# Performance work log

Measured on AMD Instinct MI355X. Metric: run time of the kernel, lower is better.

Reference implementation:

```python
import jax, jax.numpy as jnp
import numpy as np

IH = IW = 1024          # image size (iH, iW)
NMS_CAND = 1000         # dup_attrs['nms_candidates']
NMS_THR = 0.65          # dup_attrs['nms_thr']
MAX_SEGS = 100          # max_segs


def _mask_to_box(masks):
    # masks: [N, H, W] bool -> xyxy float boxes [N, 4] in pixel coords
    N, H, W = masks.shape
    rows = masks.any(axis=2)            # [N, H]
    cols = masks.any(axis=1)            # [N, W]
    x1 = jnp.argmax(cols, axis=1)
    x2 = W - jnp.argmax(cols[:, ::-1], axis=1)
    y1 = jnp.argmax(rows, axis=1)
    y2 = H - jnp.argmax(rows[:, ::-1], axis=1)
    return jnp.stack([x1, y1, x2, y2], axis=-1).astype(jnp.float32)


def _box_iou(b):
    # b: [K, 4] xyxy -> pairwise IoU [K, K]
    x1, y1, x2, y2 = b[:, 0], b[:, 1], b[:, 2], b[:, 3]
    area = (x2 - x1) * (y2 - y1)
    ix1 = jnp.maximum(x1[:, None], x1[None, :])
    iy1 = jnp.maximum(y1[:, None], y1[None, :])
    ix2 = jnp.minimum(x2[:, None], x2[None, :])
    iy2 = jnp.minimum(y2[:, None], y2[None, :])
    inter = jnp.clip(ix2 - ix1, 0.0) * jnp.clip(iy2 - iy1, 0.0)
    union = area[:, None] + area[None, :] - inter
    return inter / jnp.maximum(union, 1e-9)


def _greedy_nms_keep(iou, thr):
    # boxes assumed pre-sorted by descending score; returns keep mask [K]
    k = iou.shape[0]
    idx = jnp.arange(k)

    def body(i, keep):
        sup = keep[i] & (iou[i] > thr) & (idx > i)
        return keep & ~sup

    return jax.lax.fori_loop(0, k, body, jnp.ones((k,), dtype=bool))


def setup_inputs() -> dict:
    key = jax.random.key(0)
    k1, k2 = jax.random.split(key)
    cls_logits = jax.random.normal(k1, (300, 81), dtype=jnp.float32)
    seg_logits = jax.random.normal(k2, (300, 200, 200), dtype=jnp.float32)
    return {"cls_logits": cls_logits, "seg_logits": seg_logits}


def reference(cls_logits, seg_logits):
    N, fH, fW = seg_logits.shape
    C = cls_logits.shape[1] - 1  # last class is background/no-object

    # mask thresholding + emptiness flag (filtering replaced by score masking)
    pred_masks = seg_logits > 0                              # [N, fH, fW]
    non_empty = pred_masks.reshape(N, -1).sum(axis=1) > 0    # [N]

    # mask -> box for NMS
    boxes = _mask_to_box(pred_masks)                         # [N, 4]

    # sigmoid scoring over (feat, class); empty masks get score -1 (never picked)
    scores = jax.nn.sigmoid(cls_logits[:, :-1])              # [N, C]
    scores = jnp.where(non_empty[:, None], scores, -1.0).reshape(-1)  # [N*C]
    feat_ids = jnp.repeat(jnp.arange(N), C)                  # [N*C]
    labels = jnp.tile(jnp.arange(C), N)                      # [N*C]

    # top nms_candidates (scores sorted descending)
    k = min(NMS_CAND, N * C)
    cand_scores, cand_ids = jax.lax.top_k(scores, k)
    cand_feats = feat_ids[cand_ids]
    cand_labels = labels[cand_ids]
    cand_boxes = boxes[cand_feats]

    # batched (class-aware) NMS: offset boxes per label
    offset = cand_labels.astype(jnp.float32)[:, None] * (float(max(fH, fW)) + 1.0)
    iou = _box_iou(cand_boxes + offset)
    keep = _greedy_nms_keep(iou, NMS_THR) & (cand_scores >= 0.0)

    # keep top max_segs among survivors
    kept_scores = jnp.where(keep, cand_scores, -jnp.inf)
    sel_scores, sel = jax.lax.top_k(kept_scores, MAX_SEGS)
    sel_feats = cand_feats[sel]
    sel_labels = cand_labels[sel]

    # upsample selected mask logits to image size and threshold
    sel_logits = seg_logits[sel_feats]                       # [M, fH, fW]
    maps = jax.image.resize(sel_logits, (MAX_SEGS, IH, IW), method='bilinear')
    out_masks = maps > 0                                     # [M, iH, iW] bool
    batch_ids = jnp.zeros((MAX_SEGS,), dtype=jnp.int32)

    return sel_labels, out_masks, sel_scores, batch_ids
```

## Files before the change

kernel.cpp:

```cpp
#include <hip/hip_runtime.h>
#include <cstdint>
#include <cstddef>

typedef unsigned int u32;
typedef unsigned long long u64;
typedef float vf4 __attribute__((ext_vector_type(4)));

#define NF 300
#define NCLS 80
#define NCLS1 81
#define FH 200
#define FW 200
#define PIX 40000
#define NC 24000
#define KCAND 1000
#define CAP 4096
#define NBINS 65536
#define MAXSEG 100
#define OUT_MASK_OFF 100
#define OUT_SCORE_OFF 104857700
#define OUT_BATCH_OFF 104857800
#define NEG_BIG -3.3895313892515355e38f
#define RYC 16

#define WS_HIST      0u
#define WS_KEYS      262144u
#define WS_COLLECT   454144u
#define WS_CNT       486912u
#define WS_BOXES     486928u
#define WS_CLAB      496928u
#define WS_CFEAT     500928u
#define WS_CSCORE    504928u
#define WS_CBOX      508928u
#define WS_ROWBITS   524928u
#define WS_SELFEAT   656128u
#define WS_WTAB      656528u
#define WS_KEEP      672912u

__device__ __forceinline__ u32 ord32_r3(float f) {
  u32 b = __float_as_uint(f);
  return (b & 0x80000000u) ? ~b : (b | 0x80000000u);
}
__device__ __forceinline__ float unord32_r3(u32 o) {
  u32 b = (o & 0x80000000u) ? (o & 0x7FFFFFFFu) : ~o;
  return __uint_as_float(b);
}

__global__ void r3_init_wtab(u32* __restrict__ hist, u32* __restrict__ cnts,
                             float4* __restrict__ wtab) {
  int i = blockIdx.x * 256 + threadIdx.x;
  hist[i] = 0u;
  if (i < 4) cnts[i] = 0u;
  if (i < 1024) {
    float s = __fsub_rn(__fmul_rn((float)i + 0.5f, 0.1953125f), 0.5f);
    int j0 = (int)floorf(s);
    int j1 = j0 + 1;
    float w0 = fmaxf(0.f, __fsub_rn(1.f, fabsf(__fsub_rn(s, (float)j0))));
    float w1 = fmaxf(0.f, __fsub_rn(1.f, fabsf(__fsub_rn(s, (float)j1))));
    bool in0 = (j0 >= 0) && (j0 < FH);
    bool in1 = (j1 >= 0) && (j1 < FH);
    float tot = __fadd_rn(in0 ? w0 : 0.f, in1 ? w1 : 0.f);
    float w0n = in0 ? (w0 / tot) : 0.f;
    float w1n = in1 ? (w1 / tot) : 0.f;
    wtab[i] = make_float4(w0n, w1n, (float)max(j0, 0), (float)min(j1, FH - 1));
  }
}

__global__ void r3_boxes_scores(const float* __restrict__ seg, const float* __restrict__ cls,
                                float4* __restrict__ boxes, u64* __restrict__ keys,
                                u32* __restrict__ hist) {
  __shared__ int sminx[256], sminy[256], smaxx[256], smaxy[256];
  int n = blockIdx.x, t = threadIdx.x;
  const float4* img = (const float4*)(seg + (size_t)n * PIX);
  int minx = FW, miny = FH, maxx = -1, maxy = -1;
  for (int q = t; q < PIX / 4; q += 256) {
    float4 v = img[q];
    int p = q * 4;
    int y = p / FW;
    int x = p - y * FW;
    if (v.x > 0.f) { minx = min(minx, x);     maxx = max(maxx, x);     miny = min(miny, y); maxy = max(maxy, y); }
    if (v.y > 0.f) { minx = min(minx, x + 1); maxx = max(maxx, x + 1); miny = min(miny, y); maxy = max(maxy, y); }
    if (v.z > 0.f) { minx = min(minx, x + 2); maxx = max(maxx, x + 2); miny = min(miny, y); maxy = max(maxy, y); }
    if (v.w > 0.f) { minx = min(minx, x + 3); maxx = max(maxx, x + 3); miny = min(miny, y); maxy = max(maxy, y); }
  }
  sminx[t] = minx; sminy[t] = miny; smaxx[t] = maxx; smaxy[t] = maxy;
  __syncthreads();
  for (int s = 128; s > 0; s >>= 1) {
    if (t < s) {
      sminx[t] = min(sminx[t], sminx[t + s]);
      sminy[t] = min(sminy[t], sminy[t + s]);
      smaxx[t] = max(smaxx[t], smaxx[t + s]);
      smaxy[t] = max(smaxy[t], smaxy[t + s]);
    }
    __syncthreads();
  }
  bool ne = smaxx[0] >= 0;
  if (t == 0) {
    float4 b;
    if (ne) b = make_float4((float)sminx[0], (float)sminy[0], (float)(smaxx[0] + 1), (float)(smaxy[0] + 1));
    else    b = make_float4(0.f, 0.f, (float)FW, (float)FH);
    boxes[n] = b;
  }
  if (t < NCLS) {
    float sc;
    if (ne) {
      float lg = cls[n * NCLS1 + t];
      sc = 1.0f / (1.0f + expf(-lg));
    } else {
      sc = -1.0f;
    }
    u32 o = ord32_r3(sc);
    u32 i = (u32)(n * NCLS + t);
    keys[i] = ((u64)o << 32) | (u64)(0xFFFFFFFFu - i);
    atomicAdd(&hist[o >> 16], 1u);
  }
}

__global__ void r3_thresh(const u32* __restrict__ hist, u32* __restrict__ cnts) {
  __shared__ u32 s[1024];
  int t = threadIdx.x;
  u32 sum = 0;
  const u32* hp = hist + t * 64;
  for (int b = 0; b < 64; b++) sum += hp[b];
  s[t] = sum;
  __syncthreads();
  for (int off = 1; off < 1024; off <<= 1) {
    u32 v = s[t];
    u32 o = (t + off < 1024) ? s[t + off] : 0u;
    __syncthreads();
    s[t] = v + o;
    __syncthreads();
  }
  u32 sufnext = (t < 1023) ? s[t + 1] : 0u;
  if (s[t] >= (u32)KCAND && sufnext < (u32)KCAND) {
    u32 run = sufnext;
    u32 B = (u32)(t * 64);
    for (int b = 63; b >= 0; b--) {
      run += hist[t * 64 + b];
      if (run >= (u32)KCAND) { B = (u32)(t * 64 + b); break; }
    }
    cnts[1] = B;
  }
}

__global__ void r3_collect(const u64* __restrict__ keys, const u32* __restrict__ cnts,
                           u64* __restrict__ collect, u32* __restrict__ counter) {
  int i = blockIdx.x * 256 + threadIdx.x;
  if (i >= NC) return;
  u64 k = keys[i];
  if ((u32)(k >> 48) >= cnts[1]) {
    u32 pos = atomicAdd(counter, 1u);
    if (pos < CAP) collect[pos] = k;
  }
}

__global__ void r3_rank(const u64* __restrict__ collect, const u32* __restrict__ cnts,
                        const float4* __restrict__ boxes,
                        int* __restrict__ clab, int* __restrict__ cfeat,
                        float* __restrict__ cscore, float4* __restrict__ cbox) {
  __shared__ u64 sk[CAP];
  int M = min((int)cnts[0], CAP);
  int t = threadIdx.x;
  for (int j = t; j < M; j += 64) sk[j] = collect[j];
  __syncthreads();
  for (int j = blockIdx.x * 64 + t; j < M; j += 64 * 16) {
    u64 mykey = sk[j];
    int r = 0;
    for (int k = 0; k < M; k++) r += (sk[k] > mykey) ? 1 : 0;
    if (r < KCAND) {
      u32 idx = 0xFFFFFFFFu - (u32)(mykey & 0xFFFFFFFFull);
      int n = (int)idx / NCLS, c = (int)idx - n * NCLS;
      clab[r] = c;
      cfeat[r] = n;
      cscore[r] = unord32_r3((u32)(mykey >> 32));
      float4 b = boxes[n];
      float off = (float)c * 201.0f;
      cbox[r] = make_float4(b.x + off, b.y + off, b.z + off, b.w + off);
    }
  }
}

__global__ void r3_iou(const float4* __restrict__ cbox, u64* __restrict__ rowbits) {
  int i = blockIdx.x;
  int lane = threadIdx.x;
  float4 bi = make_float4(0.f, 0.f, 0.f, 0.f);
  float ai = 0.f;
  if (i < KCAND) { bi = cbox[i]; ai = (bi.z - bi.x) * (bi.w - bi.y); }
  for (int ch = 0; ch < 16; ch++) {
    int j = ch * 64 + lane;
    bool pred = false;
    if (i < KCAND && j < KCAND && j > i) {
      float4 bj = cbox[j];
      float aj = (bj.z - bj.x) * (bj.w - bj.y);
      float ix1 = fmaxf(bi.x, bj.x), iy1 = fmaxf(bi.y, bj.y);
      float ix2 = fminf(bi.z, bj.z), iy2 = fminf(bi.w, bj.w);
      float inter = fmaxf(ix2 - ix1, 0.f) * fmaxf(iy2 - iy1, 0.f);
      float uni = ai + aj - inter;
      float iou = inter / fmaxf(uni, 1e-9f);
      pred = iou > 0.65f;
    }
    u64 m = __ballot(pred);
    if (lane == 0) rowbits[(size_t)i * 16 + ch] = m;
  }
}

__global__ void r3_nms(const u64* __restrict__ rowbits, u64* __restrict__ keepout) {
  __shared__ u64 sup[16];
  __shared__ u64 keep[16];
  int t = threadIdx.x;
  if (t < 16) sup[t] = 0ull;
  __syncthreads();
  for (int c = 0; c < 16; c++) {
    int L = t;
    u64 r = rowbits[(size_t)(c * 64 + L) * 16 + c];
    u64 s = sup[c];
    u64 k = 0ull;
    #pragma unroll 4
    for (int b = 0; b < 64; b++) {
      u64 rb = __shfl(r, b, 64);
      if (!((s >> b) & 1ull)) { s |= rb; k |= (1ull << b); }
    }
    if (L == 0) { sup[c] = s; keep[c] = k; }
    if (L > c && L < 16) {
      u64 acc = sup[L];
      #pragma unroll
      for (int b = 0; b < 64; b++) {
        u64 v = rowbits[(size_t)(c * 64 + b) * 16 + L];
        if ((k >> b) & 1ull) acc |= v;
      }
      sup[L] = acc;
    }
    __syncthreads();
  }
  if (t < 16) keepout[t] = keep[t];
}

__global__ void r3_sel(const u64* __restrict__ keepbits, const float* __restrict__ cscore,
                       const int* __restrict__ clab, const int* __restrict__ cfeat,
                       float* __restrict__ out, int* __restrict__ selfeat) {
  __shared__ u64 sk[KCAND];
  __shared__ u64 kb[16];
  int t = threadIdx.x;
  if (t < 16) kb[t] = keepbits[t];
  __syncthreads();
  for (int j = t; j < KCAND; j += 64) {
    bool kp = ((kb[j >> 6] >> (j & 63)) & 1ull) != 0ull;
    float sc = cscore[j];
    u32 hi = (kp && sc >= 0.f) ? ord32_r3(sc) : 0u;
    sk[j] = ((u64)hi << 32) | (u64)(0xFFFFFFFFu - (u32)j);
  }
  __syncthreads();
  int j = blockIdx.x * 64 + t;
  if (j < KCAND) {
    u64 my = sk[j];
    int r = 0;
    for (int k = 0; k < KCAND; k++) r += (sk[k] > my) ? 1 : 0;
    if (r < MAXSEG) {
      u32 hi = (u32)(my >> 32);
      float oscore = (hi == 0u) ? NEG_BIG : unord32_r3(hi);
      oscore = fmaxf(oscore, NEG_BIG);
      out[r] = (float)clab[j];
      out[OUT_SCORE_OFF + r] = oscore;
      out[OUT_BATCH_OFF + r] = 0.0f;
      selfeat[r] = cfeat[j];
    }
  }
}

__global__ void __launch_bounds__(256) r3_resize(const float* __restrict__ seg,
                                                 const int* __restrict__ selfeat,
                                                 const float4* __restrict__ wtab,
                                                 float* __restrict__ outm) {
  __shared__ float srow[6][FW];
  int t = threadIdx.x;
  int yb = blockIdx.x * RYC, slot = blockIdx.y;
  int feat = selfeat[slot];
  const float* img = seg + (size_t)feat * PIX;
  float4 wxa = wtab[t * 4], wxb = wtab[t * 4 + 1], wxc = wtab[t * 4 + 2], wxd = wtab[t * 4 + 3];
  int ylo = (int)wtab[yb].z;
  int yhi = (int)wtab[yb + RYC - 1].w;
  int nr = yhi - ylo + 1;
  for (int e = t; e < nr * FW; e += 256) {
    int rr = e / FW, cc = e - rr * FW;
    srow[rr][cc] = img[(ylo + rr) * FW + cc];
  }
  __syncthreads();
  int xb = t * 4;
  int xa0 = (int)wxa.z, xa1 = (int)wxa.w;
  int xb0 = (int)wxb.z, xb1 = (int)wxb.w;
  int xc0 = (int)wxc.z, xc1 = (int)wxc.w;
  int xd0 = (int)wxd.z, xd1 = (int)wxd.w;
  float* obase = outm + (size_t)slot * 1048576 + (size_t)yb * 1024 + xb;
  #pragma unroll
  for (int r = 0; r < RYC; r++) {
    int y = yb + r;
    float4 wy = wtab[y];
    const float* r0 = srow[(int)wy.z - ylo];
    const float* r1 = srow[(int)wy.w - ylo];
    float wy0 = wy.x, wy1 = wy.y;
    float ta0 = __fmaf_rn(wy1, r1[xa0], __fmul_rn(wy0, r0[xa0]));
    float ta1 = __fmaf_rn(wy1, r1[xa1], __fmul_rn(wy0, r0[xa1]));
    float va  = __fmaf_rn(wxa.y, ta1, __fmul_rn(wxa.x, ta0));
    float tb0 = __fmaf_rn(wy1, r1[xb0], __fmul_rn(wy0, r0[xb0]));
    float tb1 = __fmaf_rn(wy1, r1[xb1], __fmul_rn(wy0, r0[xb1]));
    float vb  = __fmaf_rn(wxb.y, tb1, __fmul_rn(wxb.x, tb0));
    float tc0 = __fmaf_rn(wy1, r1[xc0], __fmul_rn(wy0, r0[xc0]));
    float tc1 = __fmaf_rn(wy1, r1[xc1], __fmul_rn(wy0, r0[xc1]));
    float vc  = __fmaf_rn(wxc.y, tc1, __fmul_rn(wxc.x, tc0));
    float td0 = __fmaf_rn(wy1, r1[xd0], __fmul_rn(wy0, r0[xd0]));
    float td1 = __fmaf_rn(wy1, r1[xd1], __fmul_rn(wy0, r0[xd1]));
    float vd  = __fmaf_rn(wxd.y, td1, __fmul_rn(wxd.x, td0));
    vf4 res;
    res.x = (va > 0.0f) ? 1.0f : 0.0f;
    res.y = (vb > 0.0f) ? 1.0f : 0.0f;
    res.z = (vc > 0.0f) ? 1.0f : 0.0f;
    res.w = (vd > 0.0f) ? 1.0f : 0.0f;
    *(vf4*)(obase + (size_t)r * 1024) = res;
  }
}

extern "C" void kernel_launch(void* const* d_in, const int* in_sizes, int n_in,
                              void* d_out, int out_size, void* d_ws, size_t ws_size,
                              hipStream_t stream) {
  const float* cls = (const float*)d_in[0];
  const float* seg = (const float*)d_in[1];
  float* out = (float*)d_out;
  char* ws = (char*)d_ws;

  u32* hist      = (u32*)(ws + WS_HIST);
  u64* keys      = (u64*)(ws + WS_KEYS);
  u64* collect   = (u64*)(ws + WS_COLLECT);
  u32* cnts      = (u32*)(ws + WS_CNT);
  float4* boxes  = (float4*)(ws + WS_BOXES);
  int* clab      = (int*)(ws + WS_CLAB);
  int* cfeat     = (int*)(ws + WS_CFEAT);
  float* cscore  = (float*)(ws + WS_CSCORE);
  float4* cbox   = (float4*)(ws + WS_CBOX);
  u64* rowbits   = (u64*)(ws + WS_ROWBITS);
  int* selfeat   = (int*)(ws + WS_SELFEAT);
  float4* wtab   = (float4*)(ws + WS_WTAB);
  u64* keepbits  = (u64*)(ws + WS_KEEP);

  r3_init_wtab<<<dim3(NBINS / 256), dim3(256), 0, stream>>>(hist, cnts, wtab);
  r3_boxes_scores<<<dim3(NF), dim3(256), 0, stream>>>(seg, cls, boxes, keys, hist);
  r3_thresh<<<dim3(1), dim3(1024), 0, stream>>>(hist, cnts);
  r3_collect<<<dim3((NC + 255) / 256), dim3(256), 0, stream>>>(keys, cnts, collect, &cnts[0]);
  r3_rank<<<dim3(16), dim3(64), 0, stream>>>(collect, cnts, boxes, clab, cfeat, cscore, cbox);
  r3_iou<<<dim3(1024), dim3(64), 0, stream>>>(cbox, rowbits);
  r3_nms<<<dim3(1), dim3(64), 0, stream>>>(rowbits, keepbits);
  r3_sel<<<dim3(16), dim3(64), 0, stream>>>(keepbits, cscore, clab, cfeat, out, selfeat);
  r3_resize<<<dim3(1024 / RYC, MAXSEG), dim3(256), 0, stream>>>(seg, selfeat, wtab, out + OUT_MASK_OFF);
}
```

Measured before the change: 642.3 us.

## Fuse NMS with selection, inline resize weights, widen small pipeline kernels

Merges the NMS and top-100 selection kernels into one 1024-thread kernel. Selection now uses a ballot and prefix-popcount compaction instead of an O(K^2) rank comparison. The bilinear weight table is dropped and weights are recomputed inline in the resize kernel, removing its table-fill work and global table loads. Collect switches to wave-aggregated atomics, rank uses 256-thread blocks so all candidates are covered in one pass, and the IoU kernel stages boxes in shared memory with four rows per block. The aim is fewer launches and less serial latency in the small control stages, at the cost of extra ALU work per resize thread.

```diff
diff --git a/kernel.cpp b/kernel.cpp
--- a/kernel.cpp
+++ b/kernel.cpp
@@ -34,8 +34,6 @@
 #define WS_CBOX      508928u
 #define WS_ROWBITS   524928u
 #define WS_SELFEAT   656128u
-#define WS_WTAB      656528u
-#define WS_KEEP      672912u
 
 __device__ __forceinline__ u32 ord32_r3(float f) {
   u32 b = __float_as_uint(f);
@@ -46,29 +44,29 @@
   return __uint_as_float(b);
 }
 
-__global__ void r3_init_wtab(u32* __restrict__ hist, u32* __restrict__ cnts,
-                             float4* __restrict__ wtab) {
+__device__ __forceinline__ float4 wcalc_r4(int i) {
+  float s = __fsub_rn(__fmul_rn((float)i + 0.5f, 0.1953125f), 0.5f);
+  int j0 = (int)floorf(s);
+  int j1 = j0 + 1;
+  float w0 = fmaxf(0.f, __fsub_rn(1.f, fabsf(__fsub_rn(s, (float)j0))));
+  float w1 = fmaxf(0.f, __fsub_rn(1.f, fabsf(__fsub_rn(s, (float)j1))));
+  bool in0 = (j0 >= 0) && (j0 < FH);
+  bool in1 = (j1 >= 0) && (j1 < FH);
+  float tot = __fadd_rn(in0 ? w0 : 0.f, in1 ? w1 : 0.f);
+  float w0n = in0 ? (w0 / tot) : 0.f;
+  float w1n = in1 ? (w1 / tot) : 0.f;
+  return make_float4(w0n, w1n, (float)max(j0, 0), (float)min(j1, FH - 1));
+}
+
+__global__ void r5_init(u32* __restrict__ hist, u32* __restrict__ cnts) {
   int i = blockIdx.x * 256 + threadIdx.x;
   hist[i] = 0u;
   if (i < 4) cnts[i] = 0u;
-  if (i < 1024) {
-    float s = __fsub_rn(__fmul_rn((float)i + 0.5f, 0.1953125f), 0.5f);
-    int j0 = (int)floorf(s);
-    int j1 = j0 + 1;
-    float w0 = fmaxf(0.f, __fsub_rn(1.f, fabsf(__fsub_rn(s, (float)j0))));
-    float w1 = fmaxf(0.f, __fsub_rn(1.f, fabsf(__fsub_rn(s, (float)j1))));
-    bool in0 = (j0 >= 0) && (j0 < FH);
-    bool in1 = (j1 >= 0) && (j1 < FH);
-    float tot = __fadd_rn(in0 ? w0 : 0.f, in1 ? w1 : 0.f);
-    float w0n = in0 ? (w0 / tot) : 0.f;
-    float w1n = in1 ? (w1 / tot) : 0.f;
-    wtab[i] = make_float4(w0n, w1n, (float)max(j0, 0), (float)min(j1, FH - 1));
-  }
-}
-
-__global__ void r3_boxes_scores(const float* __restrict__ seg, const float* __restrict__ cls,
-                                float4* __restrict__ boxes, u64* __restrict__ keys,
-                                u32* __restrict__ hist) {
+}
+
+__global__ void r5_boxes(const float* __restrict__ seg, const float* __restrict__ cls,
+                         float4* __restrict__ boxes, u64* __restrict__ keys,
+                         u32* __restrict__ hist) {
   __shared__ int sminx[256], sminy[256], smaxx[256], smaxy[256];
   int n = blockIdx.x, t = threadIdx.x;
   const float4* img = (const float4*)(seg + (size_t)n * PIX);
@@ -116,7 +114,7 @@
   }
 }
 
-__global__ void r3_thresh(const u32* __restrict__ hist, u32* __restrict__ cnts) {
+__global__ void r5_thresh(const u32* __restrict__ hist, u32* __restrict__ cnts) {
   __shared__ u32 s[1024];
   int t = threadIdx.x;
   u32 sum = 0;
@@ -143,36 +141,47 @@
   }
 }
 
-__global__ void r3_collect(const u64* __restrict__ keys, const u32* __restrict__ cnts,
+__global__ void r5_collect(const u64* __restrict__ keys, const u32* __restrict__ cnts,
                            u64* __restrict__ collect, u32* __restrict__ counter) {
   int i = blockIdx.x * 256 + threadIdx.x;
-  if (i >= NC) return;
-  u64 k = keys[i];
-  if ((u32)(k >> 48) >= cnts[1]) {
-    u32 pos = atomicAdd(counter, 1u);
+  u32 B = cnts[1];
+  bool pass = false;
+  u64 k = 0ull;
+  if (i < NC) {
+    k = keys[i];
+    pass = ((u32)(k >> 48) >= B);
+  }
+  u64 m = __ballot(pass);
+  int lane = threadIdx.x & 63;
+  u32 base = 0u;
+  if (lane == 0 && m) base = atomicAdd(counter, (u32)__popcll(m));
+  base = __shfl(base, 0, 64);
+  if (pass) {
+    u32 pos = base + (u32)__popcll(m & ((1ull << lane) - 1ull));
     if (pos < CAP) collect[pos] = k;
   }
 }
 
-__global__ void r3_rank(const u64* __restrict__ collect, const u32* __restrict__ cnts,
+__global__ void r5_rank(const u64* __restrict__ collect, const u32* __restrict__ cnts,
                         const float4* __restrict__ boxes,
                         int* __restrict__ clab, int* __restrict__ cfeat,
                         float* __restrict__ cscore, float4* __restrict__ cbox) {
   __shared__ u64 sk[CAP];
   int M = min((int)cnts[0], CAP);
   int t = threadIdx.x;
-  for (int j = t; j < M; j += 64) sk[j] = collect[j];
-  __syncthreads();
-  for (int j = blockIdx.x * 64 + t; j < M; j += 64 * 16) {
-    u64 mykey = sk[j];
+  for (int j = t; j < M; j += 256) sk[j] = collect[j];
+  __syncthreads();
+  int j = blockIdx.x * 256 + t;
+  if (j < M) {
+    u64 my = sk[j];
     int r = 0;
-    for (int k = 0; k < M; k++) r += (sk[k] > mykey) ? 1 : 0;
+    for (int k = 0; k < M; k++) r += (sk[k] > my) ? 1 : 0;
     if (r < KCAND) {
-      u32 idx = 0xFFFFFFFFu - (u32)(mykey & 0xFFFFFFFFull);
+      u32 idx = 0xFFFFFFFFu - (u32)(my & 0xFFFFFFFFull);
       int n = (int)idx / NCLS, c = (int)idx - n * NCLS;
       clab[r] = c;
       cfeat[r] = n;
-      cscore[r] = unord32_r3((u32)(mykey >> 32));
+      cscore[r] = unord32_r3((u32)(my >> 32));
       float4 b = boxes[n];
       float off = (float)c * 201.0f;
       cbox[r] = make_float4(b.x + off, b.y + off, b.z + off, b.w + off);
@@ -180,17 +189,21 @@
   }
 }
 
-__global__ void r3_iou(const float4* __restrict__ cbox, u64* __restrict__ rowbits) {
-  int i = blockIdx.x;
-  int lane = threadIdx.x;
+__global__ void r5_iou(const float4* __restrict__ cbox, u64* __restrict__ rowbits) {
+  __shared__ float4 sb[KCAND];
+  int t = threadIdx.x;
+  for (int j = t; j < KCAND; j += 256) sb[j] = cbox[j];
+  __syncthreads();
+  int w = t >> 6, lane = t & 63;
+  int i = blockIdx.x * 4 + w;
   float4 bi = make_float4(0.f, 0.f, 0.f, 0.f);
   float ai = 0.f;
-  if (i < KCAND) { bi = cbox[i]; ai = (bi.z - bi.x) * (bi.w - bi.y); }
+  if (i < KCAND) { bi = sb[i]; ai = (bi.z - bi.x) * (bi.w - bi.y); }
   for (int ch = 0; ch < 16; ch++) {
     int j = ch * 64 + lane;
     bool pred = false;
     if (i < KCAND && j < KCAND && j > i) {
-      float4 bj = cbox[j];
+      float4 bj = sb[j];
       float aj = (bj.z - bj.x) * (bj.w - bj.y);
       float ix1 = fmaxf(bi.x, bj.x), iy1 = fmaxf(bi.y, bj.y);
       float ix2 = fminf(bi.z, bj.z), iy2 = fminf(bi.w, bj.w);
@@ -204,81 +217,86 @@
   }
 }
 
-__global__ void r3_nms(const u64* __restrict__ rowbits, u64* __restrict__ keepout) {
+__global__ void r5_nms_sel(const u64* __restrict__ rowbits, const float* __restrict__ cscore,
+                           const int* __restrict__ clab, const int* __restrict__ cfeat,
+                           float* __restrict__ out, int* __restrict__ selfeat) {
   __shared__ u64 sup[16];
   __shared__ u64 keep[16];
+  __shared__ u64 sel[16];
+  __shared__ u32 pre[17];
   int t = threadIdx.x;
   if (t < 16) sup[t] = 0ull;
   __syncthreads();
   for (int c = 0; c < 16; c++) {
-    int L = t;
-    u64 r = rowbits[(size_t)(c * 64 + L) * 16 + c];
-    u64 s = sup[c];
-    u64 k = 0ull;
-    #pragma unroll 4
-    for (int b = 0; b < 64; b++) {
-      u64 rb = __shfl(r, b, 64);
-      if (!((s >> b) & 1ull)) { s |= rb; k |= (1ull << b); }
-    }
-    if (L == 0) { sup[c] = s; keep[c] = k; }
-    if (L > c && L < 16) {
-      u64 acc = sup[L];
-      #pragma unroll
+    if (t < 64) {
+      int L = t;
+      u64 r = rowbits[(size_t)(c * 64 + L) * 16 + c];
+      u64 s = sup[c];
+      u64 k = 0ull;
+      #pragma unroll 4
       for (int b = 0; b < 64; b++) {
-        u64 v = rowbits[(size_t)(c * 64 + b) * 16 + L];
-        if ((k >> b) & 1ull) acc |= v;
+        u64 rb = __shfl(r, b, 64);
+        if (!((s >> b) & 1ull)) { s |= rb; k |= (1ull << b); }
       }
-      sup[L] = acc;
+      if (L == 0) { sup[c] = s; keep[c] = k; }
+      if (L > c && L < 16) {
+        u64 acc = sup[L];
+        #pragma unroll
+        for (int b = 0; b < 64; b++) {
+          u64 v = rowbits[(size_t)(c * 64 + b) * 16 + L];
+          if ((k >> b) & 1ull) acc |= v;
+        }
+        sup[L] = acc;
+      }
     }
     __syncthreads();
   }
-  if (t < 16) keepout[t] = keep[t];
-}
-
-__global__ void r3_sel(const u64* __restrict__ keepbits, const float* __restrict__ cscore,
-                       const int* __restrict__ clab, const int* __restrict__ cfeat,
-                       float* __restrict__ out, int* __restrict__ selfeat) {
-  __shared__ u64 sk[KCAND];
-  __shared__ u64 kb[16];
-  int t = threadIdx.x;
-  if (t < 16) kb[t] = keepbits[t];
-  __syncthreads();
-  for (int j = t; j < KCAND; j += 64) {
-    bool kp = ((kb[j >> 6] >> (j & 63)) & 1ull) != 0ull;
-    float sc = cscore[j];
-    u32 hi = (kp && sc >= 0.f) ? ord32_r3(sc) : 0u;
-    sk[j] = ((u64)hi << 32) | (u64)(0xFFFFFFFFu - (u32)j);
-  }
-  __syncthreads();
-  int j = blockIdx.x * 64 + t;
-  if (j < KCAND) {
-    u64 my = sk[j];
-    int r = 0;
-    for (int k = 0; k < KCAND; k++) r += (sk[k] > my) ? 1 : 0;
+  {
+    int w = t >> 6, lane = t & 63;
+    bool s = false;
+    if (t < KCAND) {
+      bool kp = ((keep[t >> 6] >> (t & 63)) & 1ull) != 0ull;
+      s = kp && (cscore[t] >= 0.f);
+    }
+    u64 m = __ballot(s);
+    if (lane == 0) sel[w] = m;
+  }
+  __syncthreads();
+  if (t == 0) {
+    u32 acc = 0;
+    #pragma unroll
+    for (int c = 0; c < 16; c++) { pre[c] = acc; acc += (u32)__popcll(sel[c]); }
+    pre[16] = acc;
+  }
+  __syncthreads();
+  u32 nkept = pre[16];
+  if (t < KCAND) {
+    int j = t;
+    u64 w = sel[j >> 6];
+    bool s = ((w >> (j & 63)) & 1ull) != 0ull;
+    u32 below = pre[j >> 6] + (u32)__popcll(w & ((1ull << (j & 63)) - 1ull));
+    u32 r = s ? below : (nkept + (u32)j - below);
     if (r < MAXSEG) {
-      u32 hi = (u32)(my >> 32);
-      float oscore = (hi == 0u) ? NEG_BIG : unord32_r3(hi);
-      oscore = fmaxf(oscore, NEG_BIG);
       out[r] = (float)clab[j];
-      out[OUT_SCORE_OFF + r] = oscore;
+      out[OUT_SCORE_OFF + r] = s ? cscore[j] : NEG_BIG;
       out[OUT_BATCH_OFF + r] = 0.0f;
       selfeat[r] = cfeat[j];
     }
   }
 }
 
-__global__ void __launch_bounds__(256) r3_resize(const float* __restrict__ seg,
+__global__ void __launch_bounds__(256) r4_resize(const float* __restrict__ seg,
                                                  const int* __restrict__ selfeat,
-                                                 const float4* __restrict__ wtab,
                                                  float* __restrict__ outm) {
   __shared__ float srow[6][FW];
   int t = threadIdx.x;
   int yb = blockIdx.x * RYC, slot = blockIdx.y;
   int feat = selfeat[slot];
   const float* img = seg + (size_t)feat * PIX;
-  float4 wxa = wtab[t * 4], wxb = wtab[t * 4 + 1], wxc = wtab[t * 4 + 2], wxd = wtab[t * 4 + 3];
-  int ylo = (int)wtab[yb].z;
-  int yhi = (int)wtab[yb + RYC - 1].w;
+  float4 wxa = wcalc_r4(t * 4), wxb = wcalc_r4(t * 4 + 1),
+         wxc = wcalc_r4(t * 4 + 2), wxd = wcalc_r4(t * 4 + 3);
+  int ylo = (int)wcalc_r4(yb).z;
+  int yhi = (int)wcalc_r4(yb + RYC - 1).w;
   int nr = yhi - ylo + 1;
   for (int e = t; e < nr * FW; e += 256) {
     int rr = e / FW, cc = e - rr * FW;
@@ -293,8 +311,7 @@
   float* obase = outm + (size_t)slot * 1048576 + (size_t)yb * 1024 + xb;
   #pragma unroll
   for (int r = 0; r < RYC; r++) {
-    int y = yb + r;
-    float4 wy = wtab[y];
+    float4 wy = wcalc_r4(yb + r);
     const float* r0 = srow[(int)wy.z - ylo];
     const float* r1 = srow[(int)wy.w - ylo];
     float wy0 = wy.x, wy1 = wy.y;
@@ -338,16 +355,13 @@
   float4* cbox   = (float4*)(ws + WS_CBOX);
   u64* rowbits   = (u64*)(ws + WS_ROWBITS);
   int* selfeat   = (int*)(ws + WS_SELFEAT);
-  float4* wtab   = (float4*)(ws + WS_WTAB);
-  u64* keepbits  = (u64*)(ws + WS_KEEP);
-
-  r3_init_wtab<<<dim3(NBINS / 256), dim3(256), 0, stream>>>(hist, cnts, wtab);
-  r3_boxes_scores<<<dim3(NF), dim3(256), 0, stream>>>(seg, cls, boxes, keys, hist);
-  r3_thresh<<<dim3(1), dim3(1024), 0, stream>>>(hist, cnts);
-  r3_collect<<<dim3((NC + 255) / 256), dim3(256), 0, stream>>>(keys, cnts, collect, &cnts[0]);
-  r3_rank<<<dim3(16), dim3(64), 0, stream>>>(collect, cnts, boxes, clab, cfeat, cscore, cbox);
-  r3_iou<<<dim3(1024), dim3(64), 0, stream>>>(cbox, rowbits);
-  r3_nms<<<dim3(1), dim3(64), 0, stream>>>(rowbits, keepbits);
-  r3_sel<<<dim3(16), dim3(64), 0, stream>>>(keepbits, cscore, clab, cfeat, out, selfeat);
-  r3_resize<<<dim3(1024 / RYC, MAXSEG), dim3(256), 0, stream>>>(seg, selfeat, wtab, out + OUT_MASK_OFF);
-}
+
+  r5_init<<<dim3(NBINS / 256), dim3(256), 0, stream>>>(hist, cnts);
+  r5_boxes<<<dim3(NF), dim3(256), 0, stream>>>(seg, cls, boxes, keys, hist);
+  r5_thresh<<<dim3(1), dim3(1024), 0, stream>>>(hist, cnts);
+  r5_collect<<<dim3((NC + 255) / 256), dim3(256), 0, stream>>>(keys, cnts, collect, &cnts[0]);
+  r5_rank<<<dim3(16), dim3(256), 0, stream>>>(collect, cnts, boxes, clab, cfeat, cscore, cbox);
+  r5_iou<<<dim3(256), dim3(256), 0, stream>>>(cbox, rowbits);
+  r5_nms_sel<<<dim3(1), dim3(1024), 0, stream>>>(rowbits, cscore, clab, cfeat, out, selfeat);
+  r4_resize<<<dim3(1024 / RYC, MAXSEG), dim3(256), 0, stream>>>(seg, selfeat, out + OUT_MASK_OFF);
+}
```

Measured after the change: 602.7 us. -6.2%, faster.
